# Kernel tuning notes

Hardware: AMD Instinct MI355X
Metric: run time of the kernel (lower is better)

The kernel has to match this reference:

```python
import jax, jax.numpy as jnp
import numpy as np

B, CIN, COUT, H, W = 4, 256, 128, 64, 64

def conv1x1(x, w, b):
    # x: [B,C,H,W], w: [O,C], b: [O]
    return jnp.einsum('bchw,oc->bohw', x, w) + b[None, :, None, None]

def setup_inputs() -> dict:
    key = jax.random.key(0)
    ks = jax.random.split(key, 9)
    s_in = 1.0 / np.sqrt(CIN)
    s_out = 1.0 / np.sqrt(COUT)
    return {
        'x': jax.random.normal(ks[0], (B, CIN, H, W), dtype=jnp.float32),
        'w_theta': jax.random.normal(ks[1], (COUT, CIN), dtype=jnp.float32) * s_in,
        'b_theta': jax.random.normal(ks[2], (COUT,), dtype=jnp.float32) * s_in,
        'w_phi': jax.random.normal(ks[3], (COUT, CIN), dtype=jnp.float32) * s_in,
        'b_phi': jax.random.normal(ks[4], (COUT,), dtype=jnp.float32) * s_in,
        'w_g': jax.random.normal(ks[5], (COUT, CIN), dtype=jnp.float32) * s_in,
        'b_g': jax.random.normal(ks[6], (COUT,), dtype=jnp.float32) * s_in,
        'w_W': jax.random.normal(ks[7], (CIN, COUT), dtype=jnp.float32) * s_out,
        'b_W': jax.random.normal(ks[8], (CIN,), dtype=jnp.float32) * s_out,
    }

def reference(x, w_theta, b_theta, w_phi, b_phi, w_g, b_g, w_W, b_W):
    b, c, h, w = x.shape
    n = h * w
    co = w_theta.shape[0]
    theta_x = conv1x1(x, w_theta, b_theta).reshape(b, co, n).transpose(0, 2, 1)  # [B,N,Co]
    phi_x = conv1x1(x, w_phi, b_phi).reshape(b, co, n)                            # [B,Co,N]
    g_x = conv1x1(x, w_g, b_g).reshape(b, co, n).transpose(0, 2, 1)               # [B,N,Co]
    scores = jnp.einsum('bnc,bcm->bnm', theta_x, phi_x)                           # [B,N,N]
    attn = jax.nn.softmax(scores, axis=-1)
    y = jnp.einsum('bnm,bmc->bnc', attn, g_x)                                     # [B,N,Co]
    y = y.transpose(0, 2, 1).reshape(b, co, h, w)
    z = conv1x1(y, w_W, b_W) + x
    return z
```

## Files before the change

kernel.cpp:

```cpp
#include <hip/hip_runtime.h>

#define B_    4
#define C_    256
#define O_    128
#define N_    4096
#define THW   256
#define TILES 64

typedef __attribute__((ext_vector_type(8))) _Float16 f16x8;
typedef __attribute__((ext_vector_type(4))) float    f32x4;

struct __align__(8) us4 { unsigned short x, y, z, w; };

__device__ __forceinline__ float bf2f(unsigned short u) {
    unsigned v = ((unsigned)u) << 16;
    union { unsigned u; float f; } c; c.u = v; return c.f;
}
__device__ __forceinline__ unsigned short f2bf(float f) {
    union { float f; unsigned u; } c; c.f = f;
    unsigned r = c.u + 0x7fffu + ((c.u >> 16) & 1u);
    return (unsigned short)(r >> 16);
}
__device__ __forceinline__ unsigned short f2h(float f) {
    _Float16 h = (_Float16)f;
    union { _Float16 h; unsigned short s; } c; c.h = h; return c.s;
}
__device__ __forceinline__ float h2f(unsigned short s) {
    union { unsigned short s; _Float16 h; } c; c.s = s; return (float)c.h;
}

__device__ __forceinline__ void load4f(const void* base, size_t idx, int isf32, float o[4]) {
    if (isf32) {
        float4 v = *(const float4*)((const float*)base + idx);
        o[0] = v.x; o[1] = v.y; o[2] = v.z; o[3] = v.w;
    } else {
        us4 v = *(const us4*)((const unsigned short*)base + idx);
        o[0] = bf2f(v.x); o[1] = bf2f(v.y); o[2] = bf2f(v.z); o[3] = bf2f(v.w);
    }
}
__device__ __forceinline__ float load1f(const void* base, size_t idx, int isf32) {
    return isf32 ? ((const float*)base)[idx] : bf2f(((const unsigned short*)base)[idx]);
}

__global__ __launch_bounds__(256) void detect_kernel(
    const unsigned short* __restrict__ xu, int* __restrict__ flag)
{
    __shared__ int cnt;
    if (threadIdx.x == 0) cnt = 0;
    __syncthreads();
    int local = 0;
    for (int i = threadIdx.x; i < 4096; i += 256) {
        unsigned short u = xu[2 * i];
        int e = (u >> 7) & 0xFF;
        if (e == 0xFF || e >= 0x90 || (e > 0 && e <= 0x60)) local++;
    }
    atomicAdd(&cnt, local);
    __syncthreads();
    if (threadIdx.x == 0) *flag = (cnt > 1024) ? 1 : 0;
}

__global__ __launch_bounds__(512, 1) void qkv_kernel(
    const void* __restrict__ x,
    const void* __restrict__ wt, const void* __restrict__ wp,
    const void* __restrict__ wg,
    const void* __restrict__ bt, const void* __restrict__ bp,
    const void* __restrict__ bg,
    const int*  __restrict__ flag,
    unsigned short* __restrict__ thph,
    unsigned short* __restrict__ gT)
{
    const int isf32 = *flag;
    const int b  = blockIdx.y;
    const int n0 = blockIdx.x * 64;
    const int tid  = threadIdx.x;
    const int wv   = tid >> 6, lane = tid & 63;
    const int quad = lane >> 4, l16 = lane & 15;
    const int wv_n  = wv & 3;
    const int wv_jg = wv >> 2;

    __shared__ alignas(16) unsigned short smem[2 * 384 * 40];
    unsigned short (*Bs)[384 * 40] = (unsigned short(*)[384 * 40])smem;
    unsigned short (*T)[68] = (unsigned short(*)[68])smem;

    f16x8 areg[8];
    {
        int n = n0 + wv_n * 16 + l16;
        size_t xb = (size_t)b * C_ * N_ + n;
        #pragma unroll
        for (int s8 = 0; s8 < 8; s8++) {
            f16x8 fr;
            #pragma unroll
            for (int e = 0; e < 8; e++) {
                int c = s8 * 32 + quad * 8 + e;
                fr[e] = (_Float16)load1f(x, xb + (size_t)c * N_, isf32);
            }
            areg[s8] = fr;
        }
    }

    us4 wreg[2][6];
    auto loadW = [&](int s8, int slot) {
        #pragma unroll
        for (int it = 0; it < 6; it++) {
            int idx = it * 512 + tid;
            int j = idx >> 3, cg = idx & 7;
            const void* wsel = j < 128 ? wt : (j < 256 ? wp : wg);
            float v[4];
            load4f(wsel, (size_t)(j & 127) * C_ + s8 * 32 + cg * 4, isf32, v);
            us4 h;
            h.x = f2h(v[0]); h.y = f2h(v[1]); h.z = f2h(v[2]); h.w = f2h(v[3]);
            wreg[slot][it] = h;
        }
    };
    auto stageW = [&](int buf, int slot) {
        #pragma unroll
        for (int it = 0; it < 6; it++) {
            int idx = it * 512 + tid;
            int j = idx >> 3, cg = idx & 7;
            *(us4*)&Bs[buf][j * 40 + cg * 4] = wreg[slot][it];
        }
    };

    loadW(0, 0);
    loadW(1, 1);
    stageW(0, 0);

    f32x4 acc[12];
    #pragma unroll
    for (int jt = 0; jt < 12; jt++) acc[jt] = (f32x4)0.f;

    #pragma unroll
    for (int i = 0; i < 8; i++) {
        __syncthreads();
        int buf = i & 1;
        #pragma unroll
        for (int jt = 0; jt < 12; jt++) {
            f16x8 bfrag = *(const f16x8*)&Bs[buf][(wv_jg * 192 + jt * 16 + l16) * 40 + quad * 8];
            acc[jt] = __builtin_amdgcn_mfma_f32_16x16x32_f16(areg[i], bfrag, acc[jt], 0, 0, 0);
        }
        if (i + 1 < 8) {
            stageW((i + 1) & 1, (i + 1) & 1);
            if (i + 2 < 8) loadW(i + 2, i & 1);
        }
    }

    #pragma unroll
    for (int jt = 0; jt < 12; jt++) {
        int j = wv_jg * 192 + jt * 16 + l16;
        if (j < 256) {
            const void* bsel = j < 128 ? bt : bp;
            float bias = load1f(bsel, j & 127, isf32);
            #pragma unroll
            for (int r = 0; r < 4; r++) {
                int n = n0 + wv_n * 16 + quad * 4 + r;
                thph[(size_t)(b * N_ + n) * THW + j] = f2h(acc[jt][r] + bias);
            }
        }
    }
    __syncthreads();
    #pragma unroll
    for (int jt = 0; jt < 12; jt++) {
        int j = wv_jg * 192 + jt * 16 + l16;
        if (j >= 256) {
            float bias = load1f(bg, j - 256, isf32);
            #pragma unroll
            for (int r = 0; r < 4; r++) {
                int nl = wv_n * 16 + quad * 4 + r;
                T[j - 256][nl] = f2h(acc[jt][r] + bias);
            }
        }
    }
    __syncthreads();
    #pragma unroll
    for (int it = 0; it < 4; it++) {
        int idx = it * 512 + tid;
        int j = idx >> 4, ng = idx & 15;
        *(us4*)(gT + ((size_t)(b * O_ + j)) * N_ + n0 + ng * 4) = *(const us4*)&T[j][ng * 4];
    }
}

__global__ __launch_bounds__(512, 4) void attn_partial(
    const unsigned short* __restrict__ thph,
    const unsigned short* __restrict__ gT,
    unsigned short* __restrict__ partO,
    float* __restrict__ pm,
    float* __restrict__ pl,
    int S)
{
    const int b    = blockIdx.z;
    const int s_id = blockIdx.y;
    const int n0   = blockIdx.x * 128;
    const int tid  = threadIdx.x;
    const int wv   = tid >> 6, lane = tid & 63;
    const int quad = lane >> 4, l16 = lane & 15;

    const int t0 = (TILES * s_id) / S;
    const int t1 = (TILES * (s_id + 1)) / S;

    __shared__ alignas(16) unsigned short Ks[64][136];
    __shared__ alignas(16) unsigned short Gs[128][72];
    __shared__ alignas(16) unsigned short Ps[8][16][72];

    f16x8 qf[4];
    {
        int qrow = n0 + wv * 16 + l16;
        const unsigned short* qp = thph + (size_t)(b * N_ + qrow) * THW;
        for (int s = 0; s < 4; s++)
            qf[s] = *(const f16x8*)(qp + s * 32 + quad * 8);
    }

    f32x4 oacc[8];
    for (int i = 0; i < 8; i++) oacc[i] = (f32x4)0.f;
    float mstate = -INFINITY, lstate = 0.f;

    us4 kreg[4], greg[4];
    auto prefetch = [&](int mt) {
        int m0 = mt * 64;
        #pragma unroll
        for (int it = 0; it < 4; it++) {
            int l = it * 512 + tid;
            int mm = l >> 5, og = l & 31;
            kreg[it] = *(const us4*)(thph + (size_t)(b * N_ + m0 + mm) * THW + O_ + og * 4);
        }
        #pragma unroll
        for (int it = 0; it < 4; it++) {
            int l = it * 512 + tid;
            int o = l >> 4, ng = l & 15;
            greg[it] = *(const us4*)(gT + ((size_t)(b * O_ + o)) * N_ + m0 + ng * 4);
        }
    };
    prefetch(t0);

    for (int mt = t0; mt < t1; mt++) {
        __syncthreads();
        #pragma unroll
        for (int it = 0; it < 4; it++) {
            int l = it * 512 + tid;
            int mm = l >> 5, og = l & 31;
            *(us4*)&Ks[mm][og * 4] = kreg[it];
        }
        #pragma unroll
        for (int it = 0; it < 4; it++) {
            int l = it * 512 + tid;
            int o = l >> 4, ng = l & 15;
            *(us4*)&Gs[o][ng * 4] = greg[it];
        }
        __syncthreads();
        if (mt + 1 < t1) prefetch(mt + 1);

        f32x4 sacc[4];
        for (int kt = 0; kt < 4; kt++) sacc[kt] = (f32x4)0.f;
        for (int s = 0; s < 4; s++) {
            for (int kt = 0; kt < 4; kt++) {
                f16x8 kb = *(const f16x8*)&Ks[kt * 16 + l16][s * 32 + quad * 8];
                sacc[kt] = __builtin_amdgcn_mfma_f32_16x16x32_f16(kb, qf[s], sacc[kt], 0, 0, 0);
            }
        }

        float rm = fmaxf(fmaxf(fmaxf(sacc[0][0], sacc[0][1]), fmaxf(sacc[0][2], sacc[0][3])),
                         fmaxf(fmaxf(sacc[1][0], sacc[1][1]), fmaxf(sacc[1][2], sacc[1][3])));
        rm = fmaxf(rm, fmaxf(fmaxf(fmaxf(sacc[2][0], sacc[2][1]), fmaxf(sacc[2][2], sacc[2][3])),
                             fmaxf(fmaxf(sacc[3][0], sacc[3][1]), fmaxf(sacc[3][2], sacc[3][3]))));
        rm = fmaxf(rm, __shfl_xor(rm, 16));
        rm = fmaxf(rm, __shfl_xor(rm, 32));

        float mnew  = fmaxf(mstate, rm);
        float alpha = __expf(mstate - mnew);
        mstate = mnew;

        float rs = 0.f;
        #pragma unroll
        for (int kt = 0; kt < 4; kt++) {
            float p0 = __expf(sacc[kt][0] - mnew);
            float p1 = __expf(sacc[kt][1] - mnew);
            float p2 = __expf(sacc[kt][2] - mnew);
            float p3 = __expf(sacc[kt][3] - mnew);
            rs += (p0 + p1) + (p2 + p3);
            us4 pk;
            pk.x = f2h(p0); pk.y = f2h(p1); pk.z = f2h(p2); pk.w = f2h(p3);
            *(us4*)&Ps[wv][l16][kt * 16 + quad * 4] = pk;
        }
        rs += __shfl_xor(rs, 16);
        rs += __shfl_xor(rs, 32);
        lstate = lstate * alpha + rs;

        float av[4];
        #pragma unroll
        for (int r = 0; r < 4; r++) av[r] = __shfl(alpha, quad * 4 + r);
        #pragma unroll
        for (int jt = 0; jt < 8; jt++)
            #pragma unroll
            for (int r = 0; r < 4; r++) oacc[jt][r] *= av[r];

        for (int s = 0; s < 2; s++) {
            f16x8 pa = *(const f16x8*)&Ps[wv][l16][s * 32 + quad * 8];
            for (int jt = 0; jt < 8; jt++) {
                f16x8 gb = *(const f16x8*)&Gs[jt * 16 + l16][s * 32 + quad * 8];
                oacc[jt] = __builtin_amdgcn_mfma_f32_16x16x32_f16(pa, gb, oacc[jt], 0, 0, 0);
            }
        }
    }

    for (int r = 0; r < 4; r++) {
        int n = n0 + wv * 16 + quad * 4 + r;
        size_t rowb = ((size_t)(s_id * B_ + b) * N_ + n) * O_;
        for (int jt = 0; jt < 8; jt++)
            partO[rowb + jt * 16 + l16] = f2h(oacc[jt][r]);
    }
    if (quad == 0) {
        int n = n0 + wv * 16 + l16;
        pm[(size_t)(s_id * B_ + b) * N_ + n] = mstate;
        pl[(size_t)(s_id * B_ + b) * N_ + n] = lstate;
    }
}

__global__ __launch_bounds__(256) void merge_kernel(
    const unsigned short* __restrict__ partO,
    const float* __restrict__ pm, const float* __restrict__ pl,
    unsigned short* __restrict__ y,
    int S)
{
    int idx = blockIdx.x * 256 + threadIdx.x;
    int bn  = idx >> 5;
    int og  = idx & 31;
    const int BN = B_ * N_;

    float M = -INFINITY;
    for (int s = 0; s < S; s++) M = fmaxf(M, pm[(size_t)s * BN + bn]);
    float w[8];
    float L = 0.f;
    for (int s = 0; s < S; s++) {
        w[s] = __expf(pm[(size_t)s * BN + bn] - M);
        L += w[s] * pl[(size_t)s * BN + bn];
    }
    float inv = 1.0f / L;

    float a0 = 0.f, a1 = 0.f, a2 = 0.f, a3 = 0.f;
    for (int s = 0; s < S; s++) {
        us4 v = *(const us4*)(partO + ((size_t)s * BN + bn) * O_ + og * 4);
        a0 += h2f(v.x) * w[s];
        a1 += h2f(v.y) * w[s];
        a2 += h2f(v.z) * w[s];
        a3 += h2f(v.w) * w[s];
    }
    us4 r;
    r.x = f2h(a0 * inv); r.y = f2h(a1 * inv);
    r.z = f2h(a2 * inv); r.w = f2h(a3 * inv);
    *(us4*)(y + (size_t)bn * O_ + og * 4) = r;
}

__global__ __launch_bounds__(256) void out_kernel(
    const unsigned short* __restrict__ y,
    const void* __restrict__ wW,
    const void* __restrict__ bW,
    const void* __restrict__ x,
    const int*  __restrict__ flag,
    void* __restrict__ z)
{
    const int isf32 = *flag;
    const int b  = blockIdx.z;
    const int c0 = blockIdx.y * 64;
    const int n0 = blockIdx.x * 128;
    const int tid  = threadIdx.x;
    const int wv   = tid >> 6, lane = tid & 63;
    const int quad = lane >> 4, l16 = lane & 15;

    __shared__ alignas(16) unsigned short Ys[128][136];
    __shared__ alignas(16) unsigned short Ws[64][136];

    for (int it = 0; it < 16; it++) {
        int l = it * 256 + tid;
        int nn = l >> 5;
        int og = l & 31;
        us4 v = *(const us4*)(y + (size_t)(b * N_ + n0 + nn) * O_ + og * 4);
        *(us4*)&Ys[nn][og * 4] = v;
    }
    for (int it = 0; it < 8; it++) {
        int l = it * 256 + tid;
        int cc = l >> 5;
        int og = l & 31;
        float v[4];
        load4f(wW, (size_t)(c0 + cc) * O_ + og * 4, isf32, v);
        Ws[cc][og * 4 + 0] = f2h(v[0]);
        Ws[cc][og * 4 + 1] = f2h(v[1]);
        Ws[cc][og * 4 + 2] = f2h(v[2]);
        Ws[cc][og * 4 + 3] = f2h(v[3]);
    }
    __syncthreads();

    f32x4 acc[8];
    for (int i = 0; i < 8; i++) acc[i] = (f32x4)0.f;
    for (int s = 0; s < 4; s++) {
        f16x8 a = *(const f16x8*)&Ws[wv * 16 + l16][s * 32 + quad * 8];
        for (int nt = 0; nt < 8; nt++) {
            f16x8 bb = *(const f16x8*)&Ys[nt * 16 + l16][s * 32 + quad * 8];
            acc[nt] = __builtin_amdgcn_mfma_f32_16x16x32_f16(a, bb, acc[nt], 0, 0, 0);
        }
    }
    for (int r = 0; r < 4; r++) {
        int c = c0 + wv * 16 + quad * 4 + r;
        float bias = load1f(bW, c, isf32);
        for (int nt = 0; nt < 8; nt++) {
            int n = n0 + nt * 16 + l16;
            size_t idx = (size_t)(b * C_ + c) * N_ + n;
            float zv = acc[nt][r] + bias + load1f(x, idx, isf32);
            if (isf32) ((float*)z)[idx] = zv;
            else       ((unsigned short*)z)[idx] = f2bf(zv);
        }
    }
}

extern "C" void kernel_launch(void* const* d_in, const int* in_sizes, int n_in,
                              void* d_out, int out_size, void* d_ws, size_t ws_size,
                              hipStream_t stream) {
    const void* x  = d_in[0];
    const void* wt = d_in[1];
    const void* bt = d_in[2];
    const void* wp = d_in[3];
    const void* bp = d_in[4];
    const void* wg = d_in[5];
    const void* bg = d_in[6];
    const void* wW = d_in[7];
    const void* bW = d_in[8];

    const size_t base = 64 + 8388608  + 4194304 ;
    const size_t per_split = 4194304  + 131072 ;
    int S = 4;
    while (S > 1 && base + (size_t)S * per_split > ws_size) S--;

    char* p = (char*)d_ws;
    int* flag = (int*)p;                    p += 64;
    unsigned short* thph = (unsigned short*)p;  p += 8388608;
    unsigned short* gT   = (unsigned short*)p;  p += 4194304;
    unsigned short* partO = (unsigned short*)p; p += (size_t)S * 4194304;
    float* pm = (float*)p;                  p += (size_t)S * 65536;
    float* pl = (float*)p;
    unsigned short* y = gT;

    detect_kernel<<<1, 256, 0, stream>>>((const unsigned short*)x, flag);

    dim3 g1(N_ / 64, B_);
    qkv_kernel<<<g1, 512, 0, stream>>>(x, wt, wp, wg, bt, bp, bg, flag, thph, gT);

    dim3 g2(N_ / 128, S, B_);
    attn_partial<<<g2, 512, 0, stream>>>(thph, gT, partO, pm, pl, S);

    merge_kernel<<<(B_ * N_ * 32) / 256, 256, 0, stream>>>(partO, pm, pl, y, S);

    dim3 g3(N_ / 128, C_ / 64, B_);
    out_kernel<<<g3, 256, 0, stream>>>(y, wW, bW, x, flag, d_out);
}
```

Before: 216.1 us.

## Fuse split-softmax merge into output projection and halve QKV tile width

```diff
diff --git a/kernel.cpp b/kernel.cpp
--- a/kernel.cpp
+++ b/kernel.cpp
@@ -59,7 +59,7 @@
     if (threadIdx.x == 0) *flag = (cnt > 1024) ? 1 : 0;
 }
 
-__global__ __launch_bounds__(512, 1) void qkv_kernel(
+__global__ __launch_bounds__(512, 2) void qkv_kernel(
     const void* __restrict__ x,
     const void* __restrict__ wt, const void* __restrict__ wp,
     const void* __restrict__ wg,
@@ -71,16 +71,16 @@
 {
     const int isf32 = *flag;
     const int b  = blockIdx.y;
-    const int n0 = blockIdx.x * 64;
+    const int n0 = blockIdx.x * 32;
     const int tid  = threadIdx.x;
     const int wv   = tid >> 6, lane = tid & 63;
     const int quad = lane >> 4, l16 = lane & 15;
-    const int wv_n  = wv & 3;
-    const int wv_jg = wv >> 2;
+    const int wv_n  = wv & 1;
+    const int wv_jg = wv >> 1;
 
     __shared__ alignas(16) unsigned short smem[2 * 384 * 40];
     unsigned short (*Bs)[384 * 40] = (unsigned short(*)[384 * 40])smem;
-    unsigned short (*T)[68] = (unsigned short(*)[68])smem;
+    unsigned short (*T)[34] = (unsigned short(*)[34])smem;
 
     f16x8 areg[8];
     {
@@ -125,17 +125,17 @@
     loadW(1, 1);
     stageW(0, 0);
 
-    f32x4 acc[12];
+    f32x4 acc[6];
     #pragma unroll
-    for (int jt = 0; jt < 12; jt++) acc[jt] = (f32x4)0.f;
+    for (int jt = 0; jt < 6; jt++) acc[jt] = (f32x4)0.f;
 
     #pragma unroll
     for (int i = 0; i < 8; i++) {
         __syncthreads();
         int buf = i & 1;
         #pragma unroll
-        for (int jt = 0; jt < 12; jt++) {
-            f16x8 bfrag = *(const f16x8*)&Bs[buf][(wv_jg * 192 + jt * 16 + l16) * 40 + quad * 8];
+        for (int jt = 0; jt < 6; jt++) {
+            f16x8 bfrag = *(const f16x8*)&Bs[buf][(wv_jg * 96 + jt * 16 + l16) * 40 + quad * 8];
             acc[jt] = __builtin_amdgcn_mfma_f32_16x16x32_f16(areg[i], bfrag, acc[jt], 0, 0, 0);
         }
         if (i + 1 < 8) {
@@ -145,8 +145,8 @@
     }
 
     #pragma unroll
-    for (int jt = 0; jt < 12; jt++) {
-        int j = wv_jg * 192 + jt * 16 + l16;
+    for (int jt = 0; jt < 6; jt++) {
+        int j = wv_jg * 96 + jt * 16 + l16;
         if (j < 256) {
             const void* bsel = j < 128 ? bt : bp;
             float bias = load1f(bsel, j & 127, isf32);
@@ -159,8 +159,8 @@
     }
     __syncthreads();
     #pragma unroll
-    for (int jt = 0; jt < 12; jt++) {
-        int j = wv_jg * 192 + jt * 16 + l16;
+    for (int jt = 0; jt < 6; jt++) {
+        int j = wv_jg * 96 + jt * 16 + l16;
         if (j >= 256) {
             float bias = load1f(bg, j - 256, isf32);
             #pragma unroll
@@ -172,9 +172,9 @@
     }
     __syncthreads();
     #pragma unroll
-    for (int it = 0; it < 4; it++) {
+    for (int it = 0; it < 2; it++) {
         int idx = it * 512 + tid;
-        int j = idx >> 4, ng = idx & 15;
+        int j = idx >> 3, ng = idx & 7;
         *(us4*)(gT + ((size_t)(b * O_ + j)) * N_ + n0 + ng * 4) = *(const us4*)&T[j][ng * 4];
     }
 }
@@ -314,48 +314,15 @@
     }
 }
 
-__global__ __launch_bounds__(256) void merge_kernel(
+__global__ __launch_bounds__(256) void out_kernel(
     const unsigned short* __restrict__ partO,
     const float* __restrict__ pm, const float* __restrict__ pl,
-    unsigned short* __restrict__ y,
-    int S)
-{
-    int idx = blockIdx.x * 256 + threadIdx.x;
-    int bn  = idx >> 5;
-    int og  = idx & 31;
-    const int BN = B_ * N_;
-
-    float M = -INFINITY;
-    for (int s = 0; s < S; s++) M = fmaxf(M, pm[(size_t)s * BN + bn]);
-    float w[8];
-    float L = 0.f;
-    for (int s = 0; s < S; s++) {
-        w[s] = __expf(pm[(size_t)s * BN + bn] - M);
-        L += w[s] * pl[(size_t)s * BN + bn];
-    }
-    float inv = 1.0f / L;
-
-    float a0 = 0.f, a1 = 0.f, a2 = 0.f, a3 = 0.f;
-    for (int s = 0; s < S; s++) {
-        us4 v = *(const us4*)(partO + ((size_t)s * BN + bn) * O_ + og * 4);
-        a0 += h2f(v.x) * w[s];
-        a1 += h2f(v.y) * w[s];
-        a2 += h2f(v.z) * w[s];
-        a3 += h2f(v.w) * w[s];
-    }
-    us4 r;
-    r.x = f2h(a0 * inv); r.y = f2h(a1 * inv);
-    r.z = f2h(a2 * inv); r.w = f2h(a3 * inv);
-    *(us4*)(y + (size_t)bn * O_ + og * 4) = r;
-}
-
-__global__ __launch_bounds__(256) void out_kernel(
-    const unsigned short* __restrict__ y,
     const void* __restrict__ wW,
     const void* __restrict__ bW,
     const void* __restrict__ x,
     const int*  __restrict__ flag,
-    void* __restrict__ z)
+    void* __restrict__ z,
+    int S)
 {
     const int isf32 = *flag;
     const int b  = blockIdx.z;
@@ -364,16 +331,44 @@
     const int tid  = threadIdx.x;
     const int wv   = tid >> 6, lane = tid & 63;
     const int quad = lane >> 4, l16 = lane & 15;
+    const int BN = B_ * N_;
 
     __shared__ alignas(16) unsigned short Ys[128][136];
     __shared__ alignas(16) unsigned short Ws[64][136];
+    __shared__ float Winv[4][128];
+
+    if (tid < 128) {
+        int bn = b * N_ + n0 + tid;
+        float M = -INFINITY;
+        for (int s = 0; s < S; s++) M = fmaxf(M, pm[(size_t)s * BN + bn]);
+        float w[4];
+        float L = 0.f;
+        for (int s = 0; s < S; s++) {
+            w[s] = __expf(pm[(size_t)s * BN + bn] - M);
+            L += w[s] * pl[(size_t)s * BN + bn];
+        }
+        float inv = 1.0f / L;
+        for (int s = 0; s < S; s++) Winv[s][tid] = w[s] * inv;
+    }
+    __syncthreads();
 
     for (int it = 0; it < 16; it++) {
         int l = it * 256 + tid;
         int nn = l >> 5;
         int og = l & 31;
-        us4 v = *(const us4*)(y + (size_t)(b * N_ + n0 + nn) * O_ + og * 4);
-        *(us4*)&Ys[nn][og * 4] = v;
+        float a0 = 0.f, a1 = 0.f, a2 = 0.f, a3 = 0.f;
+        for (int s = 0; s < S; s++) {
+            us4 v = *(const us4*)(partO + ((size_t)(s * B_ + b) * N_ + n0 + nn) * O_ + og * 4);
+            float wv_ = Winv[s][nn];
+            a0 += h2f(v.x) * wv_;
+            a1 += h2f(v.y) * wv_;
+            a2 += h2f(v.z) * wv_;
+            a3 += h2f(v.w) * wv_;
+        }
+        Ys[nn][og * 4 + 0] = f2h(a0);
+        Ys[nn][og * 4 + 1] = f2h(a1);
+        Ys[nn][og * 4 + 2] = f2h(a2);
+        Ys[nn][og * 4 + 3] = f2h(a3);
     }
     for (int it = 0; it < 8; it++) {
         int l = it * 256 + tid;
@@ -435,18 +430,15 @@
     unsigned short* partO = (unsigned short*)p; p += (size_t)S * 4194304;
     float* pm = (float*)p;                  p += (size_t)S * 65536;
     float* pl = (float*)p;
-    unsigned short* y = gT;
 
     detect_kernel<<<1, 256, 0, stream>>>((const unsigned short*)x, flag);
 
-    dim3 g1(N_ / 64, B_);
+    dim3 g1(N_ / 32, B_);
     qkv_kernel<<<g1, 512, 0, stream>>>(x, wt, wp, wg, bt, bp, bg, flag, thph, gT);
 
     dim3 g2(N_ / 128, S, B_);
     attn_partial<<<g2, 512, 0, stream>>>(thph, gT, partO, pm, pl, S);
 
-    merge_kernel<<<(B_ * N_ * 32) / 256, 256, 0, stream>>>(partO, pm, pl, y, S);
-
     dim3 g3(N_ / 128, C_ / 64, B_);
-    out_kernel<<<g3, 256, 0, stream>>>(y, wW, bW, x, flag, d_out);
-}
+    out_kernel<<<g3, 256, 0, stream>>>(partO, pm, pl, wW, bW, x, flag, d_out, S);
+}
```

Measured after the change: 248.0 us. 14.7% more time.
